# Performance work log

Measured on AMD Instinct MI355X. Metric: run time of the kernel, lower is better.

The kernel has to match this reference:

```python
import jax, jax.numpy as jnp
import numpy as np

B, L, H, E = 4, 1024, 8, 64


def setup_inputs() -> dict:
    key = jax.random.key(0)
    kq, kk, kv = jax.random.split(key, 3)
    queries = jax.random.normal(kq, (B, L, H, E), dtype=jnp.float32)
    keys = jax.random.normal(kk, (B, L, H, E), dtype=jnp.float32)
    values = jax.random.normal(kv, (B, L, H, E), dtype=jnp.float32)
    attn_mask = jnp.zeros((1,), dtype=bool)  # unused by the module
    return {"queries": queries, "keys": keys, "values": values, "attn_mask": attn_mask}


def _spectral_interaction(queries, keys, values):
    # queries/keys/values: [B, L, H, E] (L == S here, so the torch truncation is a no-op)
    b, l, h, e = queries.shape
    qh = jnp.transpose(queries, (0, 2, 1, 3))  # [B,H,L,E]
    kh = jnp.transpose(keys[:, :l], (0, 2, 1, 3))  # [B,H,L,E]
    # cosine-similarity score matrix, exponentiated: exp(q.k / (|q||k|))
    q_norm = jnp.linalg.norm(qh, axis=-1, keepdims=True)  # [B,H,L,1]
    k_norm = jnp.linalg.norm(kh, axis=-1, keepdims=True)  # [B,H,L,1]
    dot_num = jnp.einsum('bhle,bhse->bhls', qh, kh)        # [B,H,L,L]
    dot_den = q_norm * jnp.swapaxes(k_norm, -1, -2)        # [B,H,L,L] via broadcast
    sim = jnp.exp(dot_num / dot_den)                       # [B,H,L,L]

    # FFT-domain double softmax over frequency bins
    inter_fft = jnp.fft.rfft(sim, axis=-1).real            # [B,H,L,F], F=L//2+1
    scale = 1.0 / np.sqrt(e)
    A = jax.nn.softmax(
        jnp.sum(jax.nn.softmax(scale * inter_fft, axis=-1), axis=-2),
        axis=-1,
    )                                                      # [B,H,F]  (dropout = identity in eval)
    A = A[:, :, None, :]                                   # [B,H,1,F]

    # gate the real part of the value spectrum, keep imag part, reconstruct
    vh = jnp.transpose(values[:, :l], (0, 2, 3, 1))        # [B,H,E,L]
    v_fft = jnp.fft.rfft(vh, axis=-1)                      # [B,H,E,F] complex
    Vc = jax.lax.complex(A * v_fft.real, v_fft.imag)       # [B,H,E,F]
    V = jnp.fft.irfft(Vc, n=l, axis=-1)                    # [B,H,E,L]
    return jnp.transpose(V, (0, 3, 2, 1))                  # [B,L,E,H] (matches torch permute(0,3,2,1))


def reference(queries, keys, values, attn_mask):
    # attn_mask is unused by the original forward
    return _spectral_interaction(queries, keys, values)
```

## Files before the change

### kernel.cpp

```cpp
#include <hip/hip_runtime.h>
#include <hip/hip_bf16.h>
#include <math.h>

#define B_ 4
#define L_ 1024
#define H_ 8
#define E_ 64
#define N_ 1024
#define NF_ 513
#define SCALE_ 0.125f
#define HE_ (H_ * E_)
#define ZP_ 1104

typedef _Float16 f16x8 __attribute__((ext_vector_type(8)));
typedef float f32x4 __attribute__((ext_vector_type(4)));

__device__ __forceinline__ int dr4(int x) {
    const int r = (int)(__brev((unsigned)x) >> 22);
    return ((r & 0x155) << 1) | ((r >> 1) & 0x155);
}

__device__ __forceinline__ int PD(int i) { return i + (i >> 4) + (i >> 6); }

__device__ __forceinline__ float2 cmulw(float2 v, float2 w, float dir) {
    const float wi = dir * w.y;
    return make_float2(v.x * w.x - v.y * wi, v.x * wi + v.y * w.x);
}

__device__ __forceinline__ void r4c(const float2 x0, const float2 x1,
                                    const float2 x2, const float2 x3,
                                    const float dir,
                                    float2& y0, float2& y1, float2& y2, float2& y3) {
    const float ax = x0.x + x2.x, ay = x0.y + x2.y;
    const float bx = x0.x - x2.x, by = x0.y - x2.y;
    const float cx = x1.x + x3.x, cy = x1.y + x3.y;
    const float dx = x1.x - x3.x, dy = x1.y - x3.y;
    y0 = make_float2(ax + cx, ay + cy);
    y2 = make_float2(ax - cx, ay - cy);
    y1 = make_float2(bx - dir * dy, by + dir * dx);
    y3 = make_float2(bx + dir * dy, by - dir * dx);
}

__device__ __forceinline__ void fill_tw(float2* tw, int t) {
    for (int i = t; i < 1024; i += 256) {
        float sv, cv;
        sincosf(6.283185307179586f * (float)i / 1024.0f, &sv, &cv);
        tw[PD(i)] = make_float2(cv, sv);
    }
}

__device__ __forceinline__ void fft_dit4p(float2* z, const float2* tw, int t, float dir) {
    #pragma unroll
    for (int st = 0; st < 5; ++st) {
        const int l2q = 2 * st, qs = 1 << l2q;
        const int pos = t & (qs - 1);
        const int base = ((t >> l2q) << (l2q + 2)) + pos;
        const int i0 = PD(base), i1 = PD(base + qs), i2 = PD(base + 2 * qs), i3 = PD(base + 3 * qs);
        float2 x0 = z[i0], x1 = z[i1], x2 = z[i2], x3 = z[i3];
        if (st) {
            const int step = 1 << (8 - l2q);
            const float2 w1 = tw[PD(pos * step)];
            const float2 w2 = tw[PD(2 * pos * step)];
            const float2 w3 = tw[PD(3 * pos * step)];
            x1 = cmulw(x1, w1, dir); x2 = cmulw(x2, w2, dir); x3 = cmulw(x3, w3, dir);
        }
        float2 y0, y1, y2, y3;
        r4c(x0, x1, x2, x3, dir, y0, y1, y2, y3);
        z[i0] = y0; z[i1] = y1; z[i2] = y2; z[i3] = y3;
        __syncthreads();
    }
}

__device__ __forceinline__ void fft_dif4p(float2* z, const float2* tw, int t, float dir) {
    #pragma unroll
    for (int st = 4; st >= 0; --st) {
        const int l2q = 2 * st, qs = 1 << l2q;
        const int pos = t & (qs - 1);
        const int base = ((t >> l2q) << (l2q + 2)) + pos;
        const int i0 = PD(base), i1 = PD(base + qs), i2 = PD(base + 2 * qs), i3 = PD(base + 3 * qs);
        const float2 x0 = z[i0], x1 = z[i1], x2 = z[i2], x3 = z[i3];
        float2 s0, s1, s2, s3;
        r4c(x0, x1, x2, x3, dir, s0, s1, s2, s3);
        if (st) {
            const int step = 1 << (8 - l2q);
            const float2 w1 = tw[PD(pos * step)];
            const float2 w2 = tw[PD(2 * pos * step)];
            const float2 w3 = tw[PD(3 * pos * step)];
            s1 = cmulw(s1, w1, dir); s2 = cmulw(s2, w2, dir); s3 = cmulw(s3, w3, dir);
        }
        z[i0] = s0; z[i1] = s1; z[i2] = s2; z[i3] = s3;
        __syncthreads();
    }
}

__global__ __launch_bounds__(256) void k_prep(const float* __restrict__ Q,
                                              const float* __restrict__ K,
                                              float* __restrict__ qninv,
                                              _Float16* __restrict__ Kh) {
    const int n = B_ * L_ * H_;
    const int i = blockIdx.x * 256 + threadIdx.x;
    if (i >= 2 * n) return;
    const float* p = (i < n) ? (Q + (size_t)i * E_) : (K + (size_t)(i - n) * E_);
    float ss = 0.0f;
    #pragma unroll
    for (int j = 0; j < 16; ++j) {
        const float4 v = *(const float4*)(p + j * 4);
        ss += v.x * v.x + v.y * v.y + v.z * v.z + v.w * v.w;
    }
    const float r = rsqrtf(ss);
    if (i < n) {
        qninv[i] = r;
    } else {
        _Float16* out = Kh + (size_t)(i - n) * E_;
        #pragma unroll
        for (int e = 0; e < E_; e += 8) {
            const float4 x = *(const float4*)(p + e);
            const float4 y = *(const float4*)(p + e + 4);
            f16x8 o;
            o[0] = (_Float16)(x.x * r); o[1] = (_Float16)(x.y * r);
            o[2] = (_Float16)(x.z * r); o[3] = (_Float16)(x.w * r);
            o[4] = (_Float16)(y.x * r); o[5] = (_Float16)(y.y * r);
            o[6] = (_Float16)(y.z * r); o[7] = (_Float16)(y.w * r);
            *(f16x8*)(out + e) = o;
        }
    }
}

__global__ __attribute__((amdgpu_flat_work_group_size(256, 256), amdgpu_waves_per_eu(2, 3)))
void k_qkfft(const float* __restrict__ Q,
             const _Float16* __restrict__ Kh,
             const float* __restrict__ qninv,
             float* __restrict__ G) {
    __shared__ float2 s_z[4 * ZP_];
    __shared__ float2 s_tw[ZP_];
    __shared__ float s_acc[NF_];
    __shared__ float s_red[32];

    const int t = threadIdx.x;
    const int bid = blockIdx.x;
    const int bh = bid >> 6;
    const int chunk = bid & 63;
    const int b = bh >> 3, h = bh & 7;
    const int l0 = chunk * 16;

    const int c = t & 15;
    const int g = (t >> 4) & 3;
    const int w = t >> 6;

    fill_tw(s_tw, t);
    for (int kk = t; kk < NF_; kk += 256) s_acc[kk] = 0.0f;

    const float qn = qninv[((size_t)b * L_ + l0 + c) * H_ + h];
    const float* qrow = Q + (((size_t)b * L_ + l0 + c) * H_ + h) * E_;
    f16x8 af0, af1;
    {
        const float4 x0 = *(const float4*)(qrow + g * 8);
        const float4 y0 = *(const float4*)(qrow + g * 8 + 4);
        af0[0] = (_Float16)(x0.x * qn); af0[1] = (_Float16)(x0.y * qn);
        af0[2] = (_Float16)(x0.z * qn); af0[3] = (_Float16)(x0.w * qn);
        af0[4] = (_Float16)(y0.x * qn); af0[5] = (_Float16)(y0.y * qn);
        af0[6] = (_Float16)(y0.z * qn); af0[7] = (_Float16)(y0.w * qn);
        const float4 x1 = *(const float4*)(qrow + 32 + g * 8);
        const float4 y1 = *(const float4*)(qrow + 32 + g * 8 + 4);
        af1[0] = (_Float16)(x1.x * qn); af1[1] = (_Float16)(x1.y * qn);
        af1[2] = (_Float16)(x1.z * qn); af1[3] = (_Float16)(x1.w * qn);
        af1[4] = (_Float16)(y1.x * qn); af1[5] = (_Float16)(y1.y * qn);
        af1[6] = (_Float16)(y1.z * qn); af1[7] = (_Float16)(y1.w * qn);
    }

    f32x4 acc[16];
    #pragma unroll
    for (int n = 0; n < 16; ++n) acc[n] = (f32x4){0.0f, 0.0f, 0.0f, 0.0f};

    #pragma unroll
    for (int n = 0; n < 16; ++n) {
        const int j = w * 256 + n * 16 + c;
        const int s = dr4(j);
        const f16x8* bp = (const f16x8*)(Kh + (((size_t)b * L_ + s) * H_ + h) * E_);
        const f16x8 b0 = bp[g];
        const f16x8 b1 = bp[4 + g];
        acc[n] = __builtin_amdgcn_mfma_f32_16x16x32_f16(af0, b0, acc[n], 0, 0, 0);
        acc[n] = __builtin_amdgcn_mfma_f32_16x16x32_f16(af1, b1, acc[n], 0, 0, 0);
        if ((n & 3) == 3) __builtin_amdgcn_sched_barrier(0);
    }

    #pragma unroll
    for (int n = 0; n < 16; ++n) {
        #pragma unroll
        for (int r = 0; r < 4; ++r) acc[n][r] = __expf(acc[n][r]);
    }

    const int lane = t & 63, wid = t >> 6;
    const float dir = -1.0f;

    #pragma unroll
    for (int rr = 0; rr < 2; ++rr) {
        {
            const int gq = g - 2 * rr;
            if (gq == 0 || gq == 1) {
                float2* z01 = s_z + (2 * gq) * ZP_;
                #pragma unroll
                for (int n = 0; n < 16; ++n) {
                    const int ps = PD(w * 256 + n * 16 + c);
                    z01[ps]       = make_float2(acc[n][0], acc[n][1]);
                    z01[ZP_ + ps] = make_float2(acc[n][2], acc[n][3]);
                }
            }
        }
        __syncthreads();

        #pragma unroll
        for (int st = 0; st < 5; ++st) {
            const int l2q = 2 * st, qs = 1 << l2q;
            const int pos = t & (qs - 1);
            const int base = ((t >> l2q) << (l2q + 2)) + pos;
            const int i0 = PD(base), i1 = PD(base + qs), i2 = PD(base + 2 * qs), i3 = PD(base + 3 * qs);
            float2 w1, w2, w3;
            if (st) {
                const int step = 1 << (8 - l2q);
                w1 = s_tw[PD(pos * step)];
                w2 = s_tw[PD(2 * pos * step)];
                w3 = s_tw[PD(3 * pos * step)];
            }
            #pragma unroll
            for (int q = 0; q < 4; ++q) {
                float2* z = s_z + q * ZP_;
                float2 x0 = z[i0], x1 = z[i1], x2 = z[i2], x3 = z[i3];
                if (st) { x1 = cmulw(x1, w1, dir); x2 = cmulw(x2, w2, dir); x3 = cmulw(x3, w3, dir); }
                float2 y0, y1, y2, y3;
                r4c(x0, x1, x2, x3, dir, y0, y1, y2, y3);
                z[i0] = y0; z[i1] = y1; z[i2] = y2; z[i3] = y3;
            }
            __syncthreads();
        }

        const int iT = PD(t), iTn = PD((N_ - t) & (N_ - 1));
        const int iU = PD(t + 256), iUn = PD(768 - t);
        float v[8][2], mx[8], p[8][2], pm[8], sm[8];
        #pragma unroll
        for (int q = 0; q < 4; ++q) {
            const float2* z = s_z + q * ZP_;
            const float2 X0 = z[iT], X0n = z[iTn], X1 = z[iU], X1n = z[iUn];
            const float2 DC = z[0];
            const float2 XN = z[PD(512)];
            v[2 * q][0]     = SCALE_ * 0.5f * (X0.x + X0n.x);
            v[2 * q][1]     = SCALE_ * 0.5f * (X1.x + X1n.x);
            v[2 * q + 1][0] = SCALE_ * 0.5f * (X0.y + X0n.y);
            v[2 * q + 1][1] = SCALE_ * 0.5f * (X1.y + X1n.y);
            mx[2 * q]     = SCALE_ * DC.x;
            mx[2 * q + 1] = SCALE_ * DC.y;
            pm[2 * q]     = __expf(SCALE_ * XN.x - mx[2 * q]);
            pm[2 * q + 1] = __expf(SCALE_ * XN.y - mx[2 * q + 1]);
        }
        #pragma unroll
        for (int q = 0; q < 8; ++q) {
            p[q][0] = __expf(v[q][0] - mx[q]);
            p[q][1] = __expf(v[q][1] - mx[q]);
            sm[q] = p[q][0] + p[q][1] + ((t == 0) ? pm[q] : 0.0f);
        }
        #pragma unroll
        for (int off = 32; off > 0; off >>= 1) {
            #pragma unroll
            for (int q = 0; q < 8; ++q) sm[q] += __shfl_xor(sm[q], off);
        }
        if (lane == 0) {
            #pragma unroll
            for (int q = 0; q < 8; ++q) s_red[4 * q + wid] = sm[q];
        }
        __syncthreads();
        float add0 = 0.0f, add1 = 0.0f, addm = 0.0f;
        #pragma unroll
        for (int q = 0; q < 8; ++q) {
            const float inv = 1.0f / (s_red[4 * q] + s_red[4 * q + 1] +
                                      s_red[4 * q + 2] + s_red[4 * q + 3]);
            add0 += p[q][0] * inv;
            add1 += p[q][1] * inv;
            addm += pm[q] * inv;
        }
        s_acc[t]       += add0;
        s_acc[t + 256] += add1;
        if (t == 0) s_acc[512] += addm;
        __syncthreads();
    }

    float* Gp = G + (size_t)bh * NF_;
    for (int kk = t; kk < NF_; kk += 256) atomicAdd(&Gp[kk], s_acc[kk]);
}

__global__ __launch_bounds__(256) void k_softA(const float* __restrict__ G,
                                               float* __restrict__ A) {
    __shared__ float s_red[16];
    const int bh = blockIdx.x, t = threadIdx.x;
    const float* Gp = G + (size_t)bh * NF_;
    const float g0 = Gp[t];
    const float g1 = Gp[t + 256];
    const float g2 = (t == 0) ? Gp[512] : -1e30f;
    float m = fmaxf(fmaxf(g0, g1), g2);
    #pragma unroll
    for (int off = 32; off > 0; off >>= 1) m = fmaxf(m, __shfl_xor(m, off));
    const int lane = t & 63, wid = t >> 6;
    if (lane == 0) s_red[wid] = m;
    __syncthreads();
    m = fmaxf(fmaxf(s_red[0], s_red[1]), fmaxf(s_red[2], s_red[3]));
    const float p0 = __expf(g0 - m), p1 = __expf(g1 - m);
    const float p2 = (t == 0) ? __expf(g2 - m) : 0.0f;
    float s = p0 + p1 + p2;
    #pragma unroll
    for (int off = 32; off > 0; off >>= 1) s += __shfl_xor(s, off);
    __syncthreads();
    if (lane == 0) s_red[4 + wid] = s;
    __syncthreads();
    s = s_red[4] + s_red[5] + s_red[6] + s_red[7];
    const float inv = 1.0f / s;
    float* Ap = A + (size_t)bh * NF_;
    Ap[t] = p0 * inv;
    Ap[t + 256] = p1 * inv;
    if (t == 0) Ap[512] = p2 * inv;
}

__global__ __launch_bounds__(256) void k_vfft(const float* __restrict__ V,
                                              const float* __restrict__ A,
                                              float* __restrict__ Out) {
    __shared__ float2 s_z[ZP_];
    __shared__ float2 s_w[ZP_];
    __shared__ float2 s_tw[ZP_];
    __shared__ float s_A[NF_];

    const int t = threadIdx.x;
    const int bid = blockIdx.x;
    const int bh = bid >> 5, ep = bid & 31;
    const int b = bh >> 3, h = bh & 7;
    const int e0 = ep * 2;

    fill_tw(s_tw, t);
    for (int kk = t; kk < NF_; kk += 256) s_A[kk] = A[(size_t)bh * NF_ + kk];
    #pragma unroll
    for (int jj = 0; jj < 4; ++jj) {
        const int s = jj * 256 + t;
        const float* vp = V + (((size_t)b * L_ + s) * H_ + h) * E_ + e0;
        s_z[PD(dr4(s))] = make_float2(vp[0], vp[1]);
    }
    __syncthreads();

    fft_dit4p(s_z, s_tw, t, -1.0f);

    #pragma unroll
    for (int jj = 0; jj < 4; ++jj) {
        const int k = jj * 256 + t;
        const int m = (k <= 512) ? k : (N_ - k);
        const float sgn = (k <= 512) ? 1.0f : -1.0f;
        const int mp = (N_ - m) & (N_ - 1);
        const float2 X1 = s_z[PD(m)];
        const float2 X2 = s_z[PD(mp)];
        const float reV1 = 0.5f * (X1.x + X2.x);
        const float imV1 = 0.5f * (X1.y - X2.y);
        const float reV2 = 0.5f * (X1.y + X2.y);
        const float imV2 = 0.5f * (X2.x - X1.x);
        const float a = s_A[m];
        s_w[PD(k)] = make_float2(a * reV1 - sgn * imV2, sgn * imV1 + a * reV2);
    }
    __syncthreads();

    fft_dif4p(s_w, s_tw, t, +1.0f);

    const float invN = 1.0f / (float)N_;
    #pragma unroll
    for (int jj = 0; jj < 4; ++jj) {
        const int p = jj * 256 + t;
        const int l = dr4(p);
        const float2 r = s_w[PD(p)];
        const size_t o = (((size_t)b * L_ + l) * E_ + e0) * H_ + h;
        Out[o] = r.x * invN;
        Out[o + H_] = r.y * invN;
    }
}

extern "C" void kernel_launch(void* const* d_in, const int* in_sizes, int n_in,
                              void* d_out, int out_size, void* d_ws, size_t ws_size,
                              hipStream_t stream) {
    const float* Q = (const float*)d_in[0];
    const float* K = (const float*)d_in[1];
    const float* V = (const float*)d_in[2];
    float* out = (float*)d_out;

    float* ws = (float*)d_ws;
    float* qninv   = ws;
    _Float16* Kh   = (_Float16*)(ws + B_ * L_ * H_);
    float* G       = ws + B_ * L_ * H_ + (B_ * L_ * H_ * E_) / 2;
    float* A       = G + B_ * H_ * NF_;

    hipMemsetAsync(G, 0, (size_t)B_ * H_ * NF_ * sizeof(float), stream);
    k_prep<<<(2 * B_ * L_ * H_ + 255) / 256, 256, 0, stream>>>(Q, K, qninv, Kh);
    k_qkfft<<<B_ * H_ * (L_ / 16), 256, 0, stream>>>(Q, Kh, qninv, G);
    k_softA<<<B_ * H_, 256, 0, stream>>>(G, A);
    k_vfft<<<B_ * H_ * (E_ / 2), 256, 0, stream>>>(V, A, out);
}
```

Measured before the change: 119.1 us.

## Use per-wavefront FFTs, fuse softmax into V kernel, compute Q norms inline

```diff
diff --git a/kernel.cpp b/kernel.cpp
--- a/kernel.cpp
+++ b/kernel.cpp
@@ -49,58 +49,61 @@
     }
 }
 
-__device__ __forceinline__ void fft_dit4p(float2* z, const float2* tw, int t, float dir) {
+__device__ __forceinline__ void wfft_dit4(float2* z, const float2* tw, int lane, float dir) {
     #pragma unroll
     for (int st = 0; st < 5; ++st) {
         const int l2q = 2 * st, qs = 1 << l2q;
-        const int pos = t & (qs - 1);
-        const int base = ((t >> l2q) << (l2q + 2)) + pos;
-        const int i0 = PD(base), i1 = PD(base + qs), i2 = PD(base + 2 * qs), i3 = PD(base + 3 * qs);
-        float2 x0 = z[i0], x1 = z[i1], x2 = z[i2], x3 = z[i3];
-        if (st) {
-            const int step = 1 << (8 - l2q);
-            const float2 w1 = tw[PD(pos * step)];
-            const float2 w2 = tw[PD(2 * pos * step)];
-            const float2 w3 = tw[PD(3 * pos * step)];
-            x1 = cmulw(x1, w1, dir); x2 = cmulw(x2, w2, dir); x3 = cmulw(x3, w3, dir);
-        }
-        float2 y0, y1, y2, y3;
-        r4c(x0, x1, x2, x3, dir, y0, y1, y2, y3);
-        z[i0] = y0; z[i1] = y1; z[i2] = y2; z[i3] = y3;
-        __syncthreads();
-    }
-}
-
-__device__ __forceinline__ void fft_dif4p(float2* z, const float2* tw, int t, float dir) {
+        const int step = 1 << (8 - l2q);
+        #pragma unroll
+        for (int ib = 0; ib < 4; ++ib) {
+            const int j = lane + 64 * ib;
+            const int pos = j & (qs - 1);
+            const int base = ((j >> l2q) << (l2q + 2)) + pos;
+            const int i0 = PD(base), i1 = PD(base + qs), i2 = PD(base + 2 * qs), i3 = PD(base + 3 * qs);
+            float2 x0 = z[i0], x1 = z[i1], x2 = z[i2], x3 = z[i3];
+            if (st) {
+                x1 = cmulw(x1, tw[PD(pos * step)], dir);
+                x2 = cmulw(x2, tw[PD(2 * pos * step)], dir);
+                x3 = cmulw(x3, tw[PD(3 * pos * step)], dir);
+            }
+            float2 y0, y1, y2, y3;
+            r4c(x0, x1, x2, x3, dir, y0, y1, y2, y3);
+            z[i0] = y0; z[i1] = y1; z[i2] = y2; z[i3] = y3;
+        }
+        __builtin_amdgcn_wave_barrier();
+    }
+}
+
+__device__ __forceinline__ void wfft_dif4(float2* z, const float2* tw, int lane, float dir) {
     #pragma unroll
     for (int st = 4; st >= 0; --st) {
         const int l2q = 2 * st, qs = 1 << l2q;
-        const int pos = t & (qs - 1);
-        const int base = ((t >> l2q) << (l2q + 2)) + pos;
-        const int i0 = PD(base), i1 = PD(base + qs), i2 = PD(base + 2 * qs), i3 = PD(base + 3 * qs);
-        const float2 x0 = z[i0], x1 = z[i1], x2 = z[i2], x3 = z[i3];
-        float2 s0, s1, s2, s3;
-        r4c(x0, x1, x2, x3, dir, s0, s1, s2, s3);
-        if (st) {
-            const int step = 1 << (8 - l2q);
-            const float2 w1 = tw[PD(pos * step)];
-            const float2 w2 = tw[PD(2 * pos * step)];
-            const float2 w3 = tw[PD(3 * pos * step)];
-            s1 = cmulw(s1, w1, dir); s2 = cmulw(s2, w2, dir); s3 = cmulw(s3, w3, dir);
-        }
-        z[i0] = s0; z[i1] = s1; z[i2] = s2; z[i3] = s3;
-        __syncthreads();
-    }
-}
-
-__global__ __launch_bounds__(256) void k_prep(const float* __restrict__ Q,
-                                              const float* __restrict__ K,
-                                              float* __restrict__ qninv,
+        const int step = 1 << (8 - l2q);
+        #pragma unroll
+        for (int ib = 0; ib < 4; ++ib) {
+            const int j = lane + 64 * ib;
+            const int pos = j & (qs - 1);
+            const int base = ((j >> l2q) << (l2q + 2)) + pos;
+            const int i0 = PD(base), i1 = PD(base + qs), i2 = PD(base + 2 * qs), i3 = PD(base + 3 * qs);
+            const float2 x0 = z[i0], x1 = z[i1], x2 = z[i2], x3 = z[i3];
+            float2 s0, s1, s2, s3;
+            r4c(x0, x1, x2, x3, dir, s0, s1, s2, s3);
+            if (st) {
+                s1 = cmulw(s1, tw[PD(pos * step)], dir);
+                s2 = cmulw(s2, tw[PD(2 * pos * step)], dir);
+                s3 = cmulw(s3, tw[PD(3 * pos * step)], dir);
+            }
+            z[i0] = s0; z[i1] = s1; z[i2] = s2; z[i3] = s3;
+        }
+        __builtin_amdgcn_wave_barrier();
+    }
+}
+
+__global__ __launch_bounds__(256) void k_prep(const float* __restrict__ K,
                                               _Float16* __restrict__ Kh) {
-    const int n = B_ * L_ * H_;
     const int i = blockIdx.x * 256 + threadIdx.x;
-    if (i >= 2 * n) return;
-    const float* p = (i < n) ? (Q + (size_t)i * E_) : (K + (size_t)(i - n) * E_);
+    if (i >= B_ * L_ * H_) return;
+    const float* p = K + (size_t)i * E_;
     float ss = 0.0f;
     #pragma unroll
     for (int j = 0; j < 16; ++j) {
@@ -108,33 +111,27 @@
         ss += v.x * v.x + v.y * v.y + v.z * v.z + v.w * v.w;
     }
     const float r = rsqrtf(ss);
-    if (i < n) {
-        qninv[i] = r;
-    } else {
-        _Float16* out = Kh + (size_t)(i - n) * E_;
-        #pragma unroll
-        for (int e = 0; e < E_; e += 8) {
-            const float4 x = *(const float4*)(p + e);
-            const float4 y = *(const float4*)(p + e + 4);
-            f16x8 o;
-            o[0] = (_Float16)(x.x * r); o[1] = (_Float16)(x.y * r);
-            o[2] = (_Float16)(x.z * r); o[3] = (_Float16)(x.w * r);
-            o[4] = (_Float16)(y.x * r); o[5] = (_Float16)(y.y * r);
-            o[6] = (_Float16)(y.z * r); o[7] = (_Float16)(y.w * r);
-            *(f16x8*)(out + e) = o;
-        }
+    _Float16* out = Kh + (size_t)i * E_;
+    #pragma unroll
+    for (int e = 0; e < E_; e += 8) {
+        const float4 x = *(const float4*)(p + e);
+        const float4 y = *(const float4*)(p + e + 4);
+        f16x8 o;
+        o[0] = (_Float16)(x.x * r); o[1] = (_Float16)(x.y * r);
+        o[2] = (_Float16)(x.z * r); o[3] = (_Float16)(x.w * r);
+        o[4] = (_Float16)(y.x * r); o[5] = (_Float16)(y.y * r);
+        o[6] = (_Float16)(y.z * r); o[7] = (_Float16)(y.w * r);
+        *(f16x8*)(out + e) = o;
     }
 }
 
 __global__ __attribute__((amdgpu_flat_work_group_size(256, 256), amdgpu_waves_per_eu(2, 3)))
 void k_qkfft(const float* __restrict__ Q,
              const _Float16* __restrict__ Kh,
-             const float* __restrict__ qninv,
              float* __restrict__ G) {
     __shared__ float2 s_z[4 * ZP_];
     __shared__ float2 s_tw[ZP_];
     __shared__ float s_acc[NF_];
-    __shared__ float s_red[32];
 
     const int t = threadIdx.x;
     const int bid = blockIdx.x;
@@ -146,27 +143,32 @@
     const int c = t & 15;
     const int g = (t >> 4) & 3;
     const int w = t >> 6;
+    const int lane = t & 63;
 
     fill_tw(s_tw, t);
     for (int kk = t; kk < NF_; kk += 256) s_acc[kk] = 0.0f;
 
-    const float qn = qninv[((size_t)b * L_ + l0 + c) * H_ + h];
     const float* qrow = Q + (((size_t)b * L_ + l0 + c) * H_ + h) * E_;
+    const float4 x0 = *(const float4*)(qrow + g * 8);
+    const float4 y0 = *(const float4*)(qrow + g * 8 + 4);
+    const float4 x1 = *(const float4*)(qrow + 32 + g * 8);
+    const float4 y1 = *(const float4*)(qrow + 32 + g * 8 + 4);
+    float ss = x0.x * x0.x + x0.y * x0.y + x0.z * x0.z + x0.w * x0.w
+             + y0.x * y0.x + y0.y * y0.y + y0.z * y0.z + y0.w * y0.w
+             + x1.x * x1.x + x1.y * x1.y + x1.z * x1.z + x1.w * x1.w
+             + y1.x * y1.x + y1.y * y1.y + y1.z * y1.z + y1.w * y1.w;
+    ss += __shfl_xor(ss, 16);
+    ss += __shfl_xor(ss, 32);
+    const float qn = rsqrtf(ss);
     f16x8 af0, af1;
-    {
-        const float4 x0 = *(const float4*)(qrow + g * 8);
-        const float4 y0 = *(const float4*)(qrow + g * 8 + 4);
-        af0[0] = (_Float16)(x0.x * qn); af0[1] = (_Float16)(x0.y * qn);
-        af0[2] = (_Float16)(x0.z * qn); af0[3] = (_Float16)(x0.w * qn);
-        af0[4] = (_Float16)(y0.x * qn); af0[5] = (_Float16)(y0.y * qn);
-        af0[6] = (_Float16)(y0.z * qn); af0[7] = (_Float16)(y0.w * qn);
-        const float4 x1 = *(const float4*)(qrow + 32 + g * 8);
-        const float4 y1 = *(const float4*)(qrow + 32 + g * 8 + 4);
-        af1[0] = (_Float16)(x1.x * qn); af1[1] = (_Float16)(x1.y * qn);
-        af1[2] = (_Float16)(x1.z * qn); af1[3] = (_Float16)(x1.w * qn);
-        af1[4] = (_Float16)(y1.x * qn); af1[5] = (_Float16)(y1.y * qn);
-        af1[6] = (_Float16)(y1.z * qn); af1[7] = (_Float16)(y1.w * qn);
-    }
+    af0[0] = (_Float16)(x0.x * qn); af0[1] = (_Float16)(x0.y * qn);
+    af0[2] = (_Float16)(x0.z * qn); af0[3] = (_Float16)(x0.w * qn);
+    af0[4] = (_Float16)(y0.x * qn); af0[5] = (_Float16)(y0.y * qn);
+    af0[6] = (_Float16)(y0.z * qn); af0[7] = (_Float16)(y0.w * qn);
+    af1[0] = (_Float16)(x1.x * qn); af1[1] = (_Float16)(x1.y * qn);
+    af1[2] = (_Float16)(x1.z * qn); af1[3] = (_Float16)(x1.w * qn);
+    af1[4] = (_Float16)(y1.x * qn); af1[5] = (_Float16)(y1.y * qn);
+    af1[6] = (_Float16)(y1.z * qn); af1[7] = (_Float16)(y1.w * qn);
 
     f32x4 acc[16];
     #pragma unroll
@@ -190,11 +192,17 @@
         for (int r = 0; r < 4; ++r) acc[n][r] = __expf(acc[n][r]);
     }
 
-    const int lane = t & 63, wid = t >> 6;
+    float gacc[8];
+    #pragma unroll
+    for (int ib = 0; ib < 8; ++ib) gacc[ib] = 0.0f;
+    float gN = 0.0f;
+
+    float2* zw = s_z + w * ZP_;
     const float dir = -1.0f;
 
     #pragma unroll
     for (int rr = 0; rr < 2; ++rr) {
+        __syncthreads();
         {
             const int gq = g - 2 * rr;
             if (gq == 0 || gq == 1) {
@@ -209,166 +217,135 @@
         }
         __syncthreads();
 
-        #pragma unroll
-        for (int st = 0; st < 5; ++st) {
-            const int l2q = 2 * st, qs = 1 << l2q;
-            const int pos = t & (qs - 1);
-            const int base = ((t >> l2q) << (l2q + 2)) + pos;
-            const int i0 = PD(base), i1 = PD(base + qs), i2 = PD(base + 2 * qs), i3 = PD(base + 3 * qs);
-            float2 w1, w2, w3;
-            if (st) {
-                const int step = 1 << (8 - l2q);
-                w1 = s_tw[PD(pos * step)];
-                w2 = s_tw[PD(2 * pos * step)];
-                w3 = s_tw[PD(3 * pos * step)];
-            }
-            #pragma unroll
-            for (int q = 0; q < 4; ++q) {
-                float2* z = s_z + q * ZP_;
-                float2 x0 = z[i0], x1 = z[i1], x2 = z[i2], x3 = z[i3];
-                if (st) { x1 = cmulw(x1, w1, dir); x2 = cmulw(x2, w2, dir); x3 = cmulw(x3, w3, dir); }
-                float2 y0, y1, y2, y3;
-                r4c(x0, x1, x2, x3, dir, y0, y1, y2, y3);
-                z[i0] = y0; z[i1] = y1; z[i2] = y2; z[i3] = y3;
-            }
-            __syncthreads();
-        }
-
-        const int iT = PD(t), iTn = PD((N_ - t) & (N_ - 1));
-        const int iU = PD(t + 256), iUn = PD(768 - t);
-        float v[8][2], mx[8], p[8][2], pm[8], sm[8];
-        #pragma unroll
-        for (int q = 0; q < 4; ++q) {
-            const float2* z = s_z + q * ZP_;
-            const float2 X0 = z[iT], X0n = z[iTn], X1 = z[iU], X1n = z[iUn];
-            const float2 DC = z[0];
-            const float2 XN = z[PD(512)];
-            v[2 * q][0]     = SCALE_ * 0.5f * (X0.x + X0n.x);
-            v[2 * q][1]     = SCALE_ * 0.5f * (X1.x + X1n.x);
-            v[2 * q + 1][0] = SCALE_ * 0.5f * (X0.y + X0n.y);
-            v[2 * q + 1][1] = SCALE_ * 0.5f * (X1.y + X1n.y);
-            mx[2 * q]     = SCALE_ * DC.x;
-            mx[2 * q + 1] = SCALE_ * DC.y;
-            pm[2 * q]     = __expf(SCALE_ * XN.x - mx[2 * q]);
-            pm[2 * q + 1] = __expf(SCALE_ * XN.y - mx[2 * q + 1]);
-        }
-        #pragma unroll
-        for (int q = 0; q < 8; ++q) {
-            p[q][0] = __expf(v[q][0] - mx[q]);
-            p[q][1] = __expf(v[q][1] - mx[q]);
-            sm[q] = p[q][0] + p[q][1] + ((t == 0) ? pm[q] : 0.0f);
+        wfft_dit4(zw, s_tw, lane, dir);
+
+        const float mA = SCALE_ * zw[0].x;
+        const float mB = SCALE_ * zw[0].y;
+        float pA[8], pB[8], sA = 0.0f, sB = 0.0f;
+        #pragma unroll
+        for (int ib = 0; ib < 8; ++ib) {
+            const int k = lane + 64 * ib;
+            const int kp = (N_ - k) & (N_ - 1);
+            const float2 X1 = zw[PD(k)];
+            const float2 X2 = zw[PD(kp)];
+            pA[ib] = __expf(SCALE_ * 0.5f * (X1.x + X2.x) - mA);
+            pB[ib] = __expf(SCALE_ * 0.5f * (X1.y + X2.y) - mB);
+            sA += pA[ib]; sB += pB[ib];
+        }
+        float pAN = 0.0f, pBN = 0.0f;
+        if (lane == 0) {
+            const float2 XN = zw[PD(512)];
+            pAN = __expf(SCALE_ * XN.x - mA);
+            pBN = __expf(SCALE_ * XN.y - mB);
+            sA += pAN; sB += pBN;
         }
         #pragma unroll
         for (int off = 32; off > 0; off >>= 1) {
-            #pragma unroll
-            for (int q = 0; q < 8; ++q) sm[q] += __shfl_xor(sm[q], off);
-        }
-        if (lane == 0) {
-            #pragma unroll
-            for (int q = 0; q < 8; ++q) s_red[4 * q + wid] = sm[q];
-        }
-        __syncthreads();
-        float add0 = 0.0f, add1 = 0.0f, addm = 0.0f;
-        #pragma unroll
-        for (int q = 0; q < 8; ++q) {
-            const float inv = 1.0f / (s_red[4 * q] + s_red[4 * q + 1] +
-                                      s_red[4 * q + 2] + s_red[4 * q + 3]);
-            add0 += p[q][0] * inv;
-            add1 += p[q][1] * inv;
-            addm += pm[q] * inv;
-        }
-        s_acc[t]       += add0;
-        s_acc[t + 256] += add1;
-        if (t == 0) s_acc[512] += addm;
-        __syncthreads();
-    }
+            sA += __shfl_xor(sA, off);
+            sB += __shfl_xor(sB, off);
+        }
+        const float iA = 1.0f / sA, iB = 1.0f / sB;
+        #pragma unroll
+        for (int ib = 0; ib < 8; ++ib) gacc[ib] += pA[ib] * iA + pB[ib] * iB;
+        if (lane == 0) gN += pAN * iA + pBN * iB;
+    }
+
+    #pragma unroll
+    for (int ib = 0; ib < 8; ++ib) atomicAdd(&s_acc[lane + 64 * ib], gacc[ib]);
+    if (lane == 0) atomicAdd(&s_acc[512], gN);
+    __syncthreads();
 
     float* Gp = G + (size_t)bh * NF_;
     for (int kk = t; kk < NF_; kk += 256) atomicAdd(&Gp[kk], s_acc[kk]);
 }
 
-__global__ __launch_bounds__(256) void k_softA(const float* __restrict__ G,
-                                               float* __restrict__ A) {
-    __shared__ float s_red[16];
-    const int bh = blockIdx.x, t = threadIdx.x;
-    const float* Gp = G + (size_t)bh * NF_;
-    const float g0 = Gp[t];
-    const float g1 = Gp[t + 256];
-    const float g2 = (t == 0) ? Gp[512] : -1e30f;
-    float m = fmaxf(fmaxf(g0, g1), g2);
-    #pragma unroll
-    for (int off = 32; off > 0; off >>= 1) m = fmaxf(m, __shfl_xor(m, off));
-    const int lane = t & 63, wid = t >> 6;
-    if (lane == 0) s_red[wid] = m;
-    __syncthreads();
-    m = fmaxf(fmaxf(s_red[0], s_red[1]), fmaxf(s_red[2], s_red[3]));
-    const float p0 = __expf(g0 - m), p1 = __expf(g1 - m);
-    const float p2 = (t == 0) ? __expf(g2 - m) : 0.0f;
-    float s = p0 + p1 + p2;
-    #pragma unroll
-    for (int off = 32; off > 0; off >>= 1) s += __shfl_xor(s, off);
-    __syncthreads();
-    if (lane == 0) s_red[4 + wid] = s;
-    __syncthreads();
-    s = s_red[4] + s_red[5] + s_red[6] + s_red[7];
-    const float inv = 1.0f / s;
-    float* Ap = A + (size_t)bh * NF_;
-    Ap[t] = p0 * inv;
-    Ap[t + 256] = p1 * inv;
-    if (t == 0) Ap[512] = p2 * inv;
-}
-
 __global__ __launch_bounds__(256) void k_vfft(const float* __restrict__ V,
-                                              const float* __restrict__ A,
+                                              const float* __restrict__ G,
                                               float* __restrict__ Out) {
-    __shared__ float2 s_z[ZP_];
-    __shared__ float2 s_w[ZP_];
+    __shared__ float2 s_zv[4 * ZP_];
     __shared__ float2 s_tw[ZP_];
     __shared__ float s_A[NF_];
+    __shared__ float s_red[8];
 
     const int t = threadIdx.x;
     const int bid = blockIdx.x;
-    const int bh = bid >> 5, ep = bid & 31;
+    const int bh = bid >> 3, pg = bid & 7;
     const int b = bh >> 3, h = bh & 7;
-    const int e0 = ep * 2;
+    const int w = t >> 6, lane = t & 63;
+    const int e0 = 2 * (pg * 4 + w);
 
     fill_tw(s_tw, t);
-    for (int kk = t; kk < NF_; kk += 256) s_A[kk] = A[(size_t)bh * NF_ + kk];
-    #pragma unroll
-    for (int jj = 0; jj < 4; ++jj) {
-        const int s = jj * 256 + t;
+
+    {
+        const float* Gp = G + (size_t)bh * NF_;
+        const float g0 = Gp[t];
+        const float g1 = Gp[t + 256];
+        const float g2 = (t == 0) ? Gp[512] : -1e30f;
+        float m = fmaxf(fmaxf(g0, g1), g2);
+        #pragma unroll
+        for (int off = 32; off > 0; off >>= 1) m = fmaxf(m, __shfl_xor(m, off));
+        if (lane == 0) s_red[w] = m;
+        __syncthreads();
+        m = fmaxf(fmaxf(s_red[0], s_red[1]), fmaxf(s_red[2], s_red[3]));
+        const float p0 = __expf(g0 - m), p1 = __expf(g1 - m);
+        const float p2 = (t == 0) ? __expf(g2 - m) : 0.0f;
+        float s = p0 + p1 + p2;
+        #pragma unroll
+        for (int off = 32; off > 0; off >>= 1) s += __shfl_xor(s, off);
+        __syncthreads();
+        if (lane == 0) s_red[4 + w] = s;
+        __syncthreads();
+        s = s_red[4] + s_red[5] + s_red[6] + s_red[7];
+        const float inv = 1.0f / s;
+        s_A[t] = p0 * inv;
+        s_A[t + 256] = p1 * inv;
+        if (t == 0) s_A[512] = p2 * inv;
+    }
+    __syncthreads();
+
+    float2* z = s_zv + w * ZP_;
+
+    #pragma unroll
+    for (int jb = 0; jb < 16; ++jb) {
+        const int s = lane + 64 * jb;
         const float* vp = V + (((size_t)b * L_ + s) * H_ + h) * E_ + e0;
-        s_z[PD(dr4(s))] = make_float2(vp[0], vp[1]);
-    }
-    __syncthreads();
-
-    fft_dit4p(s_z, s_tw, t, -1.0f);
-
-    #pragma unroll
-    for (int jj = 0; jj < 4; ++jj) {
-        const int k = jj * 256 + t;
-        const int m = (k <= 512) ? k : (N_ - k);
-        const float sgn = (k <= 512) ? 1.0f : -1.0f;
-        const int mp = (N_ - m) & (N_ - 1);
-        const float2 X1 = s_z[PD(m)];
-        const float2 X2 = s_z[PD(mp)];
+        z[PD(dr4(s))] = make_float2(vp[0], vp[1]);
+    }
+    __builtin_amdgcn_wave_barrier();
+
+    wfft_dit4(z, s_tw, lane, -1.0f);
+
+    #pragma unroll
+    for (int ib = 0; ib < 8; ++ib) {
+        const int k = lane + 64 * ib;
+        const int kp = (N_ - k) & (N_ - 1);
+        const int ik = PD(k), ikp = PD(kp);
+        const float2 X1 = z[ik];
+        const float2 X2 = z[ikp];
         const float reV1 = 0.5f * (X1.x + X2.x);
         const float imV1 = 0.5f * (X1.y - X2.y);
         const float reV2 = 0.5f * (X1.y + X2.y);
         const float imV2 = 0.5f * (X2.x - X1.x);
-        const float a = s_A[m];
-        s_w[PD(k)] = make_float2(a * reV1 - sgn * imV2, sgn * imV1 + a * reV2);
-    }
-    __syncthreads();
-
-    fft_dif4p(s_w, s_tw, t, +1.0f);
+        const float a = s_A[k];
+        z[ik] = make_float2(a * reV1 - imV2, imV1 + a * reV2);
+        if (kp != k)
+            z[ikp] = make_float2(a * reV1 + imV2, -imV1 + a * reV2);
+    }
+    if (lane == 0) {
+        const float2 X = z[PD(512)];
+        const float a = s_A[512];
+        z[PD(512)] = make_float2(a * X.x, a * X.y);
+    }
+    __builtin_amdgcn_wave_barrier();
+
+    wfft_dif4(z, s_tw, lane, +1.0f);
 
     const float invN = 1.0f / (float)N_;
     #pragma unroll
-    for (int jj = 0; jj < 4; ++jj) {
-        const int p = jj * 256 + t;
+    for (int jb = 0; jb < 16; ++jb) {
+        const int p = lane + 64 * jb;
         const int l = dr4(p);
-        const float2 r = s_w[PD(p)];
+        const float2 r = z[PD(p)];
         const size_t o = (((size_t)b * L_ + l) * E_ + e0) * H_ + h;
         Out[o] = r.x * invN;
         Out[o + H_] = r.y * invN;
@@ -384,14 +361,11 @@
     float* out = (float*)d_out;
 
     float* ws = (float*)d_ws;
-    float* qninv   = ws;
-    _Float16* Kh   = (_Float16*)(ws + B_ * L_ * H_);
-    float* G       = ws + B_ * L_ * H_ + (B_ * L_ * H_ * E_) / 2;
-    float* A       = G + B_ * H_ * NF_;
+    float* G     = ws;
+    _Float16* Kh = (_Float16*)(ws + B_ * H_ * NF_);
 
     hipMemsetAsync(G, 0, (size_t)B_ * H_ * NF_ * sizeof(float), stream);
-    k_prep<<<(2 * B_ * L_ * H_ + 255) / 256, 256, 0, stream>>>(Q, K, qninv, Kh);
-    k_qkfft<<<B_ * H_ * (L_ / 16), 256, 0, stream>>>(Q, Kh, qninv, G);
-    k_softA<<<B_ * H_, 256, 0, stream>>>(G, A);
-    k_vfft<<<B_ * H_ * (E_ / 2), 256, 0, stream>>>(V, A, out);
-}
+    k_prep<<<(B_ * L_ * H_ + 255) / 256, 256, 0, stream>>>(K, Kh);
+    k_qkfft<<<B_ * H_ * (L_ / 16), 256, 0, stream>>>(Q, Kh, G);
+    k_vfft<<<B_ * H_ * (E_ / 8), 256, 0, stream>>>(V, G, out);
+}
```

After: 136.4 us. 14.5% more time.
